# Kernel tuning notes

Measured on AMD Instinct MI355X. Metric: run time of the kernel, lower is better.

Reference implementation:

```python
import jax, jax.numpy as jnp
import numpy as np

E = 1024
H = 4
N = 4096


def _l2norm(x, eps=1e-8):
    n = jnp.linalg.norm(x, axis=-1, keepdims=True)
    return x / jnp.maximum(n, eps)


def mha(q, k, v, in_w, in_b, out_w, out_b):
    # torch nn.MultiheadAttention, unbatched (L, E) inputs, H heads
    d = E // H
    qp = q @ in_w[:E].T + in_b[:E]            # [Lq, E]
    kp = k @ in_w[E:2 * E].T + in_b[E:2 * E]  # [Lk, E]
    vp = v @ in_w[2 * E:].T + in_b[2 * E:]    # [Lk, E]
    qh = qp.reshape(-1, H, d).transpose(1, 0, 2)  # [H, Lq, d]
    kh = kp.reshape(-1, H, d).transpose(1, 0, 2)
    vh = vp.reshape(-1, H, d).transpose(1, 0, 2)
    scores = jnp.einsum('hqd,hkd->hqk', qh, kh) / jnp.sqrt(jnp.asarray(d, qh.dtype))
    attn = jax.nn.softmax(scores, axis=-1)
    oh = jnp.einsum('hqk,hkd->hqd', attn, vh)     # [H, Lq, d]
    o = oh.transpose(1, 0, 2).reshape(-1, E)
    return o @ out_w.T + out_b


def setup_inputs() -> dict:
    key = jax.random.key(0)
    ks = jax.random.split(key, 20)
    f = lambda k, shape, s=1.0: jax.random.normal(k, shape, dtype=jnp.float32) * s
    inp = {
        'local_feat': _l2norm(f(ks[0], (N, E))),
        'global_feat': _l2norm(f(ks[1], (N, E))),
        'text_feat': _l2norm(f(ks[2], (N, E))),
        'pos_emb_local': f(ks[3], (E,), E ** -0.5),
        'pos_emb_global': f(ks[4], (E,), E ** -0.5),
        'fc_w': f(ks[5], (E, E), 0.02), 'fc_b': f(ks[6], (E,), 0.02),
        'lg_in_w': f(ks[7], (3 * E, E), 0.02), 'lg_in_b': f(ks[8], (3 * E,), 0.02),
        'lg_out_w': f(ks[9], (E, E), 0.02), 'lg_out_b': f(ks[10], (E,), 0.02),
        'vt_in_w': f(ks[11], (3 * E, E), 0.02), 'vt_in_b': f(ks[12], (3 * E,), 0.02),
        'vt_out_w': f(ks[13], (E, E), 0.02), 'vt_out_b': f(ks[14], (E,), 0.02),
        'ml_in_w': f(ks[15], (3 * E, E), 0.02), 'ml_in_b': f(ks[16], (3 * E,), 0.02),
        'ml_out_w': f(ks[17], (E, E), 0.02), 'ml_out_b': f(ks[18], (E,), 0.02),
        'quantity': 512,
    }
    return inp


def reference(local_feat, global_feat, text_feat, pos_emb_local, pos_emb_global,
              fc_w, fc_b, lg_in_w, lg_in_b, lg_out_w, lg_out_b,
              vt_in_w, vt_in_b, vt_out_w, vt_out_b,
              ml_in_w, ml_in_b, ml_out_w, ml_out_b, quantity):
    lf = local_feat + pos_emb_local
    gf = global_feat + pos_emb_global
    # local_global
    local_global = mha(lf, gf, gf, lg_in_w, lg_in_b, lg_out_w, lg_out_b) + lf
    # fusion_fc on text (applied fresh in textual_local, textual_global, repeat_text)
    tf = text_feat @ fc_w.T + fc_b
    # textual_local / textual_global (shared fusion_visual_textual weights)
    text_local = mha(tf, lf, lf, vt_in_w, vt_in_b, vt_out_w, vt_out_b) + lf
    text_global = mha(tf, gf, gf, vt_in_w, vt_in_b, vt_out_w, vt_out_b) + tf
    # middle_layer fusions (shared weights)
    gt_gl = mha(local_global, text_global, text_global, ml_in_w, ml_in_b, ml_out_w, ml_out_b)
    gl_lt = mha(text_local, local_global, local_global, ml_in_w, ml_in_b, ml_out_w, ml_out_b)
    full = mha(gl_lt, gt_gl, gt_gl, ml_in_w, ml_in_b, ml_out_w, ml_out_b)
    fusion = mha(tf, full, full, ml_in_w, ml_in_b, ml_out_w, ml_out_b) * tf
    # per-sample cosine-similarity matrices (batched replacement of the .item() loops)
    Q = quantity
    B = N // Q
    ff = _l2norm(fusion.reshape(B, Q, E))
    lb = _l2norm(local_feat.reshape(B, Q, E))
    logits = jnp.einsum('bqe,bke->bqk', ff, lb)  # [B, Q, Q]
    return logits
```

## Files before the change

### kernel.cpp

```cpp
#include <hip/hip_runtime.h>
#include <hip/hip_bf16.h>


typedef __attribute__((ext_vector_type(8))) short short8;
typedef __attribute__((ext_vector_type(4))) float f32x4;
typedef unsigned long long ull;
typedef long long ll;

namespace {
constexpr int NTOK = 4096;
constexpr int EMB  = 1024;
constexpr int QTY  = 512;
}

__device__ __forceinline__ float bf2f(unsigned short u) {
    union { float f; unsigned int i; } x; x.i = ((unsigned int)u) << 16; return x.f;
}
__device__ __forceinline__ unsigned short f2bf(float f) {
    union { float f; unsigned int i; } x; x.f = f;
    unsigned int r = x.i + 0x7fffu + ((x.i >> 16) & 1u);
    return (unsigned short)(r >> 16);
}

#define GLOAD_LDS16(g, l) __builtin_amdgcn_global_load_lds( \
    (const __attribute__((address_space(1))) void*)(g),     \
    (__attribute__((address_space(3))) void*)(l), 16, 0, 0)

template<int SPLITS, int OUTM>
__global__ __launch_bounds__(256)
void gemm_mfma(const unsigned short* __restrict__ Ah, const unsigned short* __restrict__ Al,
               int lda, ll sAz,
               const unsigned short* __restrict__ Bh, const unsigned short* __restrict__ Bl,
               int ldb, ll sBz,
               void* __restrict__ Cp, void* __restrict__ Clp,
               int ldc, ll sCz,
               int K, float alpha, const float* __restrict__ bias, int biasRow,
               const unsigned short* __restrict__ resH, const unsigned short* __restrict__ resL,
               ll sRz, int resMode)
{
    constexpr int NTILES = (SPLITS == 3 ? 4 : (SPLITS == 2 ? 3 : 2));
    constexpr int TSZ = 128 * 32;
    __shared__ unsigned short lds[NTILES * TSZ];
    const int tid  = threadIdx.x;
    const int brow = blockIdx.y * 128;
    const int bcol = blockIdx.x * 128;
    const ll   z   = blockIdx.z;
    Ah += z * sAz; Bh += z * sBz;
    if constexpr (SPLITS == 3) Al += z * sAz;
    if constexpr (SPLITS >= 2) Bl += z * sBz;

    const int lane = tid & 63;
    const int wv = tid >> 6, wr = wv >> 1, wc = wv & 1;
    const int l15 = lane & 15, l4 = lane >> 4;

    f32x4 acc[4][4];
    #pragma unroll
    for (int m = 0; m < 4; ++m)
        #pragma unroll
        for (int n = 0; n < 4; ++n) acc[m][n] = (f32x4){0.f, 0.f, 0.f, 0.f};

    for (int k0 = 0; k0 < K; k0 += 32) {
        #pragma unroll
        for (int i = 0; i < 2; ++i) {
            int idx = tid + i * 256;
            int row = idx >> 2;
            int kc  = (idx & 3) ^ ((row >> 1) & 3);
            GLOAD_LDS16(Ah + (ull)(brow + row) * lda + k0 + kc * 8, &lds[idx * 8]);
            GLOAD_LDS16(Bh + (ull)(bcol + row) * ldb + k0 + kc * 8, &lds[TSZ + idx * 8]);
            if constexpr (SPLITS >= 2)
                GLOAD_LDS16(Bl + (ull)(bcol + row) * ldb + k0 + kc * 8, &lds[2 * TSZ + idx * 8]);
            if constexpr (SPLITS == 3)
                GLOAD_LDS16(Al + (ull)(brow + row) * lda + k0 + kc * 8, &lds[3 * TSZ + idx * 8]);
        }
        __syncthreads();

        short8 ah[4], bh[4], bl2[4], al2[4];
        #pragma unroll
        for (int m = 0; m < 4; ++m) {
            int rr = wr * 64 + m * 16 + l15;
            int sl = l4 ^ ((rr >> 1) & 3);
            int off = rr * 32 + sl * 8;
            ah[m] = *(const short8*)&lds[off];
            if constexpr (SPLITS == 3) al2[m] = *(const short8*)&lds[3 * TSZ + off];
        }
        #pragma unroll
        for (int n = 0; n < 4; ++n) {
            int rr = wc * 64 + n * 16 + l15;
            int sl = l4 ^ ((rr >> 1) & 3);
            int off = rr * 32 + sl * 8;
            bh[n] = *(const short8*)&lds[TSZ + off];
            if constexpr (SPLITS >= 2) bl2[n] = *(const short8*)&lds[2 * TSZ + off];
        }
        #pragma unroll
        for (int m = 0; m < 4; ++m)
            #pragma unroll
            for (int n = 0; n < 4; ++n) {
                acc[m][n] = __builtin_amdgcn_mfma_f32_16x16x32_bf16(ah[m], bh[n], acc[m][n], 0, 0, 0);
                if constexpr (SPLITS >= 2)
                    acc[m][n] = __builtin_amdgcn_mfma_f32_16x16x32_bf16(ah[m], bl2[n], acc[m][n], 0, 0, 0);
                if constexpr (SPLITS == 3)
                    acc[m][n] = __builtin_amdgcn_mfma_f32_16x16x32_bf16(al2[m], bh[n], acc[m][n], 0, 0, 0);
            }
        __syncthreads();
    }

    float* Cf = (float*)Cp + z * sCz;
    unsigned short* Ch = (unsigned short*)Cp + z * sCz;
    unsigned short* Cl = (unsigned short*)Clp + z * sCz;
    const unsigned short* rH = resH + z * sRz;
    const unsigned short* rL = resL + z * sRz;
    const int rowB = brow + wr * 64 + l4 * 4;
    const int colB = bcol + wc * 64 + l15;
    #pragma unroll
    for (int n = 0; n < 4; ++n) {
        int col = colB + n * 16;
        #pragma unroll
        for (int m = 0; m < 4; ++m) {
            #pragma unroll
            for (int r = 0; r < 4; ++r) {
                int row = rowB + m * 16 + r;
                ull ci = (ull)row * ldc + col;
                float v = acc[m][n][r] * alpha;
                if (bias) v += biasRow ? bias[row] : bias[col];
                if (resMode == 1)      v += bf2f(rH[ci]) + bf2f(rL[ci]);
                else if (resMode == 2) v *= bf2f(rH[ci]) + bf2f(rL[ci]);
                if constexpr (OUTM == 0)      Cf[ci] = v;
                else if constexpr (OUTM == 1) Ch[ci] = f2bf(v);
                else {
                    unsigned short h = f2bf(v);
                    Ch[ci] = h;
                    Cl[ci] = f2bf(v - bf2f(h));
                }
            }
        }
    }
}

__global__ __launch_bounds__(256)
void gemm_qkproj(const unsigned short* a0, const unsigned short* a1,
                 const unsigned short* a2, const unsigned short* a3,
                 const unsigned short* __restrict__ W,
                 unsigned short* __restrict__ QK,
                 const float* __restrict__ bias)
{
    constexpr int TSZ = 128 * 32;
    __shared__ unsigned short lds[2 * TSZ];
    const int tid  = threadIdx.x;
    const int brow = blockIdx.y * 128;
    const int bcol = blockIdx.x * 128;
    const int z = blockIdx.z;
    const int j = z & 1, bb = z >> 1;
    const unsigned short* Ah = (z == 0) ? a0 : (z == 1) ? a1 : (z == 2) ? a2 : a3;
    const unsigned short* Bh = W + (ull)j * EMB * EMB;
    unsigned short* C = QK + (ull)bb * NTOK * 2048 + j * 1024;
    const float* bi = bias + j * 1024;

    const int lane = tid & 63;
    const int wv = tid >> 6, wr = wv >> 1, wc = wv & 1;
    const int l15 = lane & 15, l4 = lane >> 4;

    f32x4 acc[4][4];
    #pragma unroll
    for (int m = 0; m < 4; ++m)
        #pragma unroll
        for (int n = 0; n < 4; ++n) acc[m][n] = (f32x4){0.f, 0.f, 0.f, 0.f};

    for (int k0 = 0; k0 < EMB; k0 += 32) {
        #pragma unroll
        for (int i = 0; i < 2; ++i) {
            int idx = tid + i * 256;
            int row = idx >> 2;
            int kc  = (idx & 3) ^ ((row >> 1) & 3);
            GLOAD_LDS16(Ah + (ull)(brow + row) * EMB + k0 + kc * 8, &lds[idx * 8]);
            GLOAD_LDS16(Bh + (ull)(bcol + row) * EMB + k0 + kc * 8, &lds[TSZ + idx * 8]);
        }
        __syncthreads();

        short8 ah[4], bh[4];
        #pragma unroll
        for (int m = 0; m < 4; ++m) {
            int rr = wr * 64 + m * 16 + l15;
            int sl = l4 ^ ((rr >> 1) & 3);
            ah[m] = *(const short8*)&lds[rr * 32 + sl * 8];
        }
        #pragma unroll
        for (int n = 0; n < 4; ++n) {
            int rr = wc * 64 + n * 16 + l15;
            int sl = l4 ^ ((rr >> 1) & 3);
            bh[n] = *(const short8*)&lds[TSZ + rr * 32 + sl * 8];
        }
        #pragma unroll
        for (int m = 0; m < 4; ++m)
            #pragma unroll
            for (int n = 0; n < 4; ++n)
                acc[m][n] = __builtin_amdgcn_mfma_f32_16x16x32_bf16(ah[m], bh[n], acc[m][n], 0, 0, 0);
        __syncthreads();
    }

    const int rowB = brow + wr * 64 + l4 * 4;
    const int colB = bcol + wc * 64 + l15;
    #pragma unroll
    for (int n = 0; n < 4; ++n) {
        int col = colB + n * 16;
        float bv = bi[col];
        #pragma unroll
        for (int m = 0; m < 4; ++m)
            #pragma unroll
            for (int r = 0; r < 4; ++r) {
                int row = rowB + m * 16 + r;
                C[(ull)row * 2048 + col] = f2bf(acc[m][n][r] + bv);
            }
    }
}

template<int NSPLIT>
__global__ __launch_bounds__(512)
void flash_attn(const unsigned short* __restrict__ QK,
                const unsigned short* __restrict__ VT,
                unsigned short* __restrict__ Opart, float* __restrict__ ml,
                unsigned short* __restrict__ attH)
{
    constexpr int KVB = 64;
    constexpr int NTILE = (NTOK / NSPLIT) / KVB;
    __shared__ unsigned short Kt[2][KVB * 256];
    __shared__ unsigned short Vt[2][256 * KVB];

    const int tid = threadIdx.x;
    const int w = tid >> 6, lane = tid & 63;
    const int l15 = lane & 15, l4 = lane >> 4;
    const int qt = blockIdx.x, sp = blockIdx.y;
    const int zb = blockIdx.z, b = zb >> 2, h = zb & 3;
    const int qrow = qt * 128 + w * 16 + l15;
    const int kv0 = sp * (NTOK / NSPLIT);
    const unsigned short* QKb = QK + (ull)b * NTOK * 2048;
    const unsigned short* VTb = VT + (ull)b * 1024 * 4096;

    short8 qreg[8];
    {
        const unsigned short* qp = QKb + (ull)qrow * 2048 + h * 256;
        #pragma unroll
        for (int c = 0; c < 8; ++c) {
            short8 x = *(const short8*)&qp[c * 32 + l4 * 8];
            #pragma unroll
            for (int j = 0; j < 8; ++j)
                x[j] = (short)f2bf(bf2f((unsigned short)x[j]) * 0.0625f);
            qreg[c] = x;
        }
    }

    f32x4 oacc[16];
    #pragma unroll
    for (int dn = 0; dn < 16; ++dn) oacc[dn] = (f32x4){0.f, 0.f, 0.f, 0.f};
    float m_r = -1e30f, l_r = 0.f;

    auto stage = [&](int t, int buf) {
        int base = kv0 + t * KVB;
        #pragma unroll
        for (int i = 0; i < 4; ++i) {
            int s = tid + i * 512;
            int r = s >> 5, c = s & 31;
            int c0 = c ^ (r & 7);
            GLOAD_LDS16(QKb + (ull)(base + r) * 2048 + 1024 + h * 256 + c0 * 8,
                        &Kt[buf][s * 8]);
        }
        #pragma unroll
        for (int i = 0; i < 4; ++i) {
            int s = tid + i * 512;
            int r = s >> 3, c = s & 7;
            int c0 = c ^ (r & 7);
            GLOAD_LDS16(VTb + (ull)(h * 256 + r) * 4096 + base + c0 * 8,
                        &Vt[buf][s * 8]);
        }
    };

    stage(0, 0);
    for (int t = 0; t < NTILE; ++t) {
        if (t + 1 < NTILE) {
            stage(t + 1, (t + 1) & 1);
            asm volatile("s_waitcnt vmcnt(8)");
        } else {
            asm volatile("s_waitcnt vmcnt(0)");
        }
        __builtin_amdgcn_s_barrier();

        const unsigned short* Kb = Kt[t & 1];
        const unsigned short* Vb = Vt[t & 1];

        f32x4 sacc[4];
        #pragma unroll
        for (int fk = 0; fk < 4; ++fk) sacc[fk] = (f32x4){0.f, 0.f, 0.f, 0.f};
        #pragma unroll
        for (int fk = 0; fk < 4; ++fk) {
            int r = fk * 16 + l15;
            int rx = r & 7;
            #pragma unroll
            for (int c = 0; c < 8; ++c) {
                int ch = (4 * c + l4) ^ rx;
                short8 kf = *(const short8*)&Kb[r * 256 + ch * 8];
                sacc[fk] = __builtin_amdgcn_mfma_f32_16x16x32_bf16(kf, qreg[c], sacc[fk], 0, 0, 0);
            }
        }

        float tm = sacc[0][0];
        #pragma unroll
        for (int fk = 0; fk < 4; ++fk)
            #pragma unroll
            for (int rr = 0; rr < 4; ++rr) tm = fmaxf(tm, sacc[fk][rr]);
        tm = fmaxf(tm, __shfl_xor(tm, 16));
        tm = fmaxf(tm, __shfl_xor(tm, 32));

        bool nomax = __all(tm <= m_r);
        float mnew = nomax ? m_r : fmaxf(m_r, tm);
        if (!nomax) {
            float corr = __expf(m_r - mnew);
            float c4[4];
            #pragma unroll
            for (int r = 0; r < 4; ++r) c4[r] = __shfl(corr, l4 * 4 + r);
            #pragma unroll
            for (int dn = 0; dn < 16; ++dn)
                #pragma unroll
                for (int r = 0; r < 4; ++r) oacc[dn][r] *= c4[r];
            l_r *= corr;
            m_r = mnew;
        }

        float p[16]; float ls = 0.f;
        #pragma unroll
        for (int fk = 0; fk < 4; ++fk)
            #pragma unroll
            for (int rr = 0; rr < 4; ++rr) {
                float e = __expf(sacc[fk][rr] - m_r);
                p[fk * 4 + rr] = e; ls += e;
            }
        ls += __shfl_xor(ls, 16);
        ls += __shfl_xor(ls, 32);
        l_r += ls;

        unsigned int W[4][2];
        #pragma unroll
        for (int f = 0; f < 4; ++f)
            #pragma unroll
            for (int pp = 0; pp < 2; ++pp)
                W[f][pp] = (unsigned int)f2bf(p[f * 4 + 2 * pp]) |
                           ((unsigned int)f2bf(p[f * 4 + 2 * pp + 1]) << 16);

        const int sbase = l15 + ((l4 & 1) << 5);
        const bool hi = (l4 >> 1) & 1;
        #pragma unroll
        for (int kvc = 0; kvc < 2; ++kvc) {
            unsigned int a0 = (unsigned int)__shfl((int)W[2 * kvc][0], sbase);
            unsigned int a1 = (unsigned int)__shfl((int)W[2 * kvc][1], sbase);
            unsigned int a2 = (unsigned int)__shfl((int)W[2 * kvc][0], sbase + 16);
            unsigned int a3 = (unsigned int)__shfl((int)W[2 * kvc][1], sbase + 16);
            unsigned int b0 = (unsigned int)__shfl((int)W[2 * kvc + 1][0], sbase);
            unsigned int b1 = (unsigned int)__shfl((int)W[2 * kvc + 1][1], sbase);
            unsigned int b2 = (unsigned int)__shfl((int)W[2 * kvc + 1][0], sbase + 16);
            unsigned int b3 = (unsigned int)__shfl((int)W[2 * kvc + 1][1], sbase + 16);
            union { unsigned int u[4]; short8 s8; } pa;
            pa.u[0] = hi ? b0 : a0; pa.u[1] = hi ? b1 : a1;
            pa.u[2] = hi ? b2 : a2; pa.u[3] = hi ? b3 : a3;

            #pragma unroll
            for (int dn = 0; dn < 16; ++dn) {
                int row = dn * 16 + l15;
                int ch = (kvc * 4 + l4) ^ (row & 7);
                short8 vf = *(const short8*)&Vb[row * 64 + ch * 8];
                oacc[dn] = __builtin_amdgcn_mfma_f32_16x16x32_bf16(pa.s8, vf, oacc[dn], 0, 0, 0);
            }
        }
        __builtin_amdgcn_s_barrier();
    }

    float inv = 1.f / l_r;
    float i4[4];
    #pragma unroll
    for (int r = 0; r < 4; ++r) i4[r] = __shfl(inv, l4 * 4 + r);

    if constexpr (NSPLIT == 2) {
        unsigned short* Ob = Opart + (((ull)b * 2 + sp) * 4 + h) * NTOK * 256;
        #pragma unroll
        for (int dn = 0; dn < 16; ++dn) {
            int d = dn * 16 + l15;
            #pragma unroll
            for (int r = 0; r < 4; ++r) {
                int q = qt * 128 + w * 16 + l4 * 4 + r;
                Ob[(ull)q * 256 + d] = f2bf(oacc[dn][r] * i4[r]);
            }
        }
        if (l4 == 0) {
            float2* mlp = (float2*)ml + (((ull)b * 2 + sp) * 4 + h) * NTOK + qrow;
            *mlp = make_float2(m_r, l_r);
        }
    } else {
        unsigned short* Ob = attH + (ull)b * NTOK * EMB;
        #pragma unroll
        for (int dn = 0; dn < 16; ++dn) {
            int d = dn * 16 + l15;
            #pragma unroll
            for (int r = 0; r < 4; ++r) {
                int q = qt * 128 + w * 16 + l4 * 4 + r;
                Ob[(ull)q * EMB + h * 256 + d] = f2bf(oacc[dn][r] * i4[r]);
            }
        }
    }
}

__global__ __launch_bounds__(256)
void flash_combine(const unsigned short* __restrict__ Opart, const float* __restrict__ ml,
                   unsigned short* __restrict__ attH)
{
    const int bx = blockIdx.x;
    const int b = bx >> 12, q = bx & 4095;
    const int t = threadIdx.x;
    const int h = t >> 6, d4 = (t & 63) * 4;

    float2 m0 = ((const float2*)ml)[(((ull)b * 2 + 0) * 4 + h) * NTOK + q];
    float2 m1 = ((const float2*)ml)[(((ull)b * 2 + 1) * 4 + h) * NTOK + q];
    float ms = fmaxf(m0.x, m1.x);
    float w0 = __expf(m0.x - ms) * m0.y;
    float w1 = __expf(m1.x - ms) * m1.y;
    float inv = 1.f / (w0 + w1);
    w0 *= inv; w1 *= inv;

    ushort4 o0 = *(const ushort4*)&Opart[((((ull)b * 2 + 0) * 4 + h) * NTOK + q) * 256 + d4];
    ushort4 o1 = *(const ushort4*)&Opart[((((ull)b * 2 + 1) * 4 + h) * NTOK + q) * 256 + d4];
    ushort4 ho;
    ho.x = f2bf(w0 * bf2f(o0.x) + w1 * bf2f(o1.x));
    ho.y = f2bf(w0 * bf2f(o0.y) + w1 * bf2f(o1.y));
    ho.z = f2bf(w0 * bf2f(o0.z) + w1 * bf2f(o1.z));
    ho.w = f2bf(w0 * bf2f(o0.w) + w1 * bf2f(o1.w));
    *(ushort4*)&attH[(ull)b * NTOK * EMB + (ull)q * EMB + h * 256 + d4] = ho;
}

template<bool F32IN>
__global__ __launch_bounds__(256)
void l2norm_rows(const float* __restrict__ inF, const unsigned short* __restrict__ inH,
                 const unsigned short* __restrict__ inL,
                 unsigned short* __restrict__ oH, unsigned short* __restrict__ oL)
{
    const ull row = blockIdx.x;
    const int t = threadIdx.x;
    const int lane = t & 63, wid = t >> 6;
    __shared__ float red[4];

    float v[4];
    if constexpr (F32IN) {
        float4 x = *(const float4*)&inF[row * EMB + t * 4];
        v[0] = x.x; v[1] = x.y; v[2] = x.z; v[3] = x.w;
    } else {
        ushort4 hh = *(const ushort4*)&inH[row * EMB + t * 4];
        ushort4 ll2 = *(const ushort4*)&inL[row * EMB + t * 4];
        v[0] = bf2f(hh.x) + bf2f(ll2.x); v[1] = bf2f(hh.y) + bf2f(ll2.y);
        v[2] = bf2f(hh.z) + bf2f(ll2.z); v[3] = bf2f(hh.w) + bf2f(ll2.w);
    }
    float ss = v[0] * v[0] + v[1] * v[1] + v[2] * v[2] + v[3] * v[3];
    #pragma unroll
    for (int o = 32; o > 0; o >>= 1) ss += __shfl_down(ss, o);
    if (lane == 0) red[wid] = ss;
    __syncthreads();
    ss = red[0] + red[1] + red[2] + red[3];

    float inv = 1.f / fmaxf(sqrtf(ss), 1e-8f);
    ushort4 ho, lo;
    float s0 = v[0] * inv, s1 = v[1] * inv, s2 = v[2] * inv, s3 = v[3] * inv;
    ho.x = f2bf(s0); lo.x = f2bf(s0 - bf2f(ho.x));
    ho.y = f2bf(s1); lo.y = f2bf(s1 - bf2f(ho.y));
    ho.z = f2bf(s2); lo.z = f2bf(s2 - bf2f(ho.z));
    ho.w = f2bf(s3); lo.w = f2bf(s3 - bf2f(ho.w));
    *(ushort4*)&oH[row * EMB + t * 4] = ho;
    *(ushort4*)&oL[row * EMB + t * 4] = lo;
}

__global__ __launch_bounds__(256)
void add_pos_pair(const float* __restrict__ in, const float* __restrict__ pos,
                  unsigned short* __restrict__ oH, unsigned short* __restrict__ oL)
{
    ull i = ((ull)blockIdx.x * 256 + threadIdx.x) * 4;
    float4 a = *(const float4*)&in[i];
    float4 p = *(const float4*)&pos[(int)(i & (EMB - 1))];
    float w[4] = { a.x + p.x, a.y + p.y, a.z + p.z, a.w + p.w };
    ushort4 ho, lo;
    ho.x = f2bf(w[0]); lo.x = f2bf(w[0] - bf2f(ho.x));
    ho.y = f2bf(w[1]); lo.y = f2bf(w[1] - bf2f(ho.y));
    ho.z = f2bf(w[2]); lo.z = f2bf(w[2] - bf2f(ho.z));
    ho.w = f2bf(w[3]); lo.w = f2bf(w[3] - bf2f(ho.w));
    *(ushort4*)&oH[i] = ho;
    *(ushort4*)&oL[i] = lo;
}

__global__ __launch_bounds__(256)
void split_pair(const float* __restrict__ in, unsigned short* __restrict__ oH,
                unsigned short* __restrict__ oL)
{
    ull i = ((ull)blockIdx.x * 256 + threadIdx.x) * 4;
    float4 a = *(const float4*)&in[i];
    float w[4] = { a.x, a.y, a.z, a.w };
    ushort4 ho, lo;
    ho.x = f2bf(w[0]); lo.x = f2bf(w[0] - bf2f(ho.x));
    ho.y = f2bf(w[1]); lo.y = f2bf(w[1] - bf2f(ho.y));
    ho.z = f2bf(w[2]); lo.z = f2bf(w[2] - bf2f(ho.z));
    ho.w = f2bf(w[3]); lo.w = f2bf(w[3] - bf2f(ho.w));
    *(ushort4*)&oH[i] = ho;
    *(ushort4*)&oL[i] = lo;
}

__global__ __launch_bounds__(256)
void cast_bf16(const float* __restrict__ in, unsigned short* __restrict__ out)
{
    ull i = ((ull)blockIdx.x * 256 + threadIdx.x) * 4;
    float4 a = *(const float4*)&in[i];
    ushort4 ho;
    ho.x = f2bf(a.x); ho.y = f2bf(a.y); ho.z = f2bf(a.z); ho.w = f2bf(a.w);
    *(ushort4*)&out[i] = ho;
}

namespace {

template<int S, int O>
inline void G(dim3 grid,
              const unsigned short* Ah, const unsigned short* Al, int lda, ll sAz,
              const unsigned short* Bh, const unsigned short* Bl, int ldb, ll sBz,
              void* Ch, void* Cl, int ldc, ll sCz,
              int K, float alpha, const float* bias, int biasRow,
              const unsigned short* rh, const unsigned short* rl, ll sRz, int rm,
              hipStream_t st)
{
    gemm_mfma<S, O><<<grid, dim3(256), 0, st>>>(Ah, Al, lda, sAz, Bh, Bl, ldb, sBz,
                                                Ch, Cl, ldc, sCz, K, alpha, bias, biasRow,
                                                rh, rl, sRz, rm);
}

struct Bufs {
    unsigned short *Ph[6], *Pl[6];
    unsigned short *ATTh, *QK, *VT, *Wih, *Woh, *Wol, *Opart;
    float *ml;
};

void run_mha(int batch,
             const unsigned short* qh, ll sQ,
             const unsigned short* kh, ll sK,
             const float* in_w, const float* in_b,
             const float* out_w, const float* out_b,
             unsigned short* dsth, unsigned short* dstl,
             const unsigned short* resh, const unsigned short* resl, ll sR, int resMode,
             const Bufs& B, bool convW, hipStream_t s)
{
    const ull EE = (ull)EMB * EMB;
    const ll  TE = (ll)NTOK * EMB;
    const ll  VTBS = (ll)1024 * 4096;
    if (convW) {
        cast_bf16<<<3 * EE / 1024, 256, 0, s>>>(in_w, B.Wih);
        split_pair<<<EE / 1024, 256, 0, s>>>(out_w, B.Woh, B.Wol);
    }
    gemm_qkproj<<<dim3(8, 32, 2 * batch), 256, 0, s>>>(
        qh, kh, qh + sQ, kh + sK, B.Wih, B.QK, in_b);
    G<1, 1>(dim3(32, 8, batch), B.Wih + 2 * EE, nullptr, EMB, 0, kh, nullptr, EMB, sK,
            B.VT, nullptr, 4096, VTBS, EMB, 1.f, in_b + 2 * EMB, 1, nullptr, nullptr, 0, 0, s);

    if (batch == 1) {
        flash_attn<2><<<dim3(32, 2, 4), 512, 0, s>>>(B.QK, B.VT, B.Opart, B.ml, B.ATTh);
        flash_combine<<<NTOK, 256, 0, s>>>(B.Opart, B.ml, B.ATTh);
    } else {
        flash_attn<1><<<dim3(32, 1, 4 * batch), 512, 0, s>>>(B.QK, B.VT, B.Opart, B.ml, B.ATTh);
    }

    G<2, 2>(dim3(8, 32, batch), B.ATTh, nullptr, EMB, TE, B.Woh, B.Wol, EMB, 0,
            dsth, dstl, EMB, 2 * TE, EMB, 1.f, out_b, 0, resh, resl, sR, resMode, s);
}

}

extern "C" void kernel_launch(void* const* d_in, const int* in_sizes, int n_in,
                              void* d_out, int out_size, void* d_ws, size_t ws_size,
                              hipStream_t stream) {
    const float* local_feat  = (const float*)d_in[0];
    const float* global_feat = (const float*)d_in[1];
    const float* text_feat   = (const float*)d_in[2];
    const float* pos_l       = (const float*)d_in[3];
    const float* pos_g       = (const float*)d_in[4];
    const float* fc_w        = (const float*)d_in[5];
    const float* fc_b        = (const float*)d_in[6];
    const float* lg_in_w     = (const float*)d_in[7];
    const float* lg_in_b     = (const float*)d_in[8];
    const float* lg_out_w    = (const float*)d_in[9];
    const float* lg_out_b    = (const float*)d_in[10];
    const float* vt_in_w     = (const float*)d_in[11];
    const float* vt_in_b     = (const float*)d_in[12];
    const float* vt_out_w    = (const float*)d_in[13];
    const float* vt_out_b    = (const float*)d_in[14];
    const float* ml_in_w     = (const float*)d_in[15];
    const float* ml_in_b     = (const float*)d_in[16];
    const float* ml_out_w    = (const float*)d_in[17];
    const float* ml_out_b    = (const float*)d_in[18];
    float* out = (float*)d_out;

    const ull TE = (ull)NTOK * EMB;
    const ull EE = (ull)EMB * EMB;
    unsigned short* w = (unsigned short*)d_ws;
    Bufs B;
    for (int i = 0; i < 6; ++i) { B.Ph[i] = w + (2 * i) * TE; B.Pl[i] = w + (2 * i + 1) * TE; }
    B.ATTh  = w + 12 * TE;
    B.QK    = w + 14 * TE;
    B.VT    = w + 18 * TE;
    B.Opart = w + 20 * TE;
    B.ml    = (float*)(w + 24 * TE);
    B.Wih   = w + 25 * TE;
    B.Woh   = B.Wih + 3 * EE;
    B.Wol   = B.Woh + EE;

    add_pos_pair<<<TE / 1024, 256, 0, stream>>>(local_feat, pos_l, B.Ph[0], B.Pl[0]);
    add_pos_pair<<<TE / 1024, 256, 0, stream>>>(global_feat, pos_g, B.Ph[1], B.Pl[1]);

    split_pair<<<TE / 1024, 256, 0, stream>>>(text_feat, B.QK, B.QK + TE);
    split_pair<<<EE / 1024, 256, 0, stream>>>(fc_w, B.Woh, B.Wol);
    G<3, 2>(dim3(EMB / 128, NTOK / 128), B.QK, B.QK + TE, EMB, 0, B.Woh, B.Wol, EMB, 0,
            B.Ph[2], B.Pl[2], EMB, 0, EMB, 1.f, fc_b, 0, nullptr, nullptr, 0, 0, stream);

    const ll T2 = (ll)2 * TE, T4 = (ll)4 * TE;
    run_mha(1, B.Ph[0], 0, B.Ph[1], 0, lg_in_w, lg_in_b, lg_out_w, lg_out_b,
            B.Ph[3], B.Pl[3], B.Ph[0], B.Pl[0], 0, 1, B, true, stream);
    run_mha(2, B.Ph[2], 0, B.Ph[0], T2, vt_in_w, vt_in_b, vt_out_w, vt_out_b,
            B.Ph[4], B.Pl[4], B.Ph[0], B.Pl[0], T4, 1, B, true, stream);
    run_mha(2, B.Ph[3], T2, B.Ph[5], -T4, ml_in_w, ml_in_b, ml_out_w, ml_out_b,
            B.Ph[0], B.Pl[0], nullptr, nullptr, 0, 0, B, true, stream);
    run_mha(1, B.Ph[1], 0, B.Ph[0], 0, ml_in_w, ml_in_b, ml_out_w, ml_out_b,
            B.Ph[3], B.Pl[3], nullptr, nullptr, 0, 0, B, false, stream);
    run_mha(1, B.Ph[2], 0, B.Ph[3], 0, ml_in_w, ml_in_b, ml_out_w, ml_out_b,
            B.Ph[4], B.Pl[4], B.Ph[2], B.Pl[2], 0, 2, B, false, stream);

    l2norm_rows<false><<<NTOK, 256, 0, stream>>>(nullptr, B.Ph[4], B.Pl[4], B.Ph[4], B.Pl[4]);
    l2norm_rows<true ><<<NTOK, 256, 0, stream>>>(local_feat, nullptr, nullptr, B.Ph[5], B.Pl[5]);

    G<3, 0>(dim3(QTY / 128, QTY / 128, 8),
            B.Ph[4], B.Pl[4], EMB, (ll)QTY * EMB,
            B.Ph[5], B.Pl[5], EMB, (ll)QTY * EMB,
            out, nullptr, QTY, (ll)QTY * QTY,
            EMB, 1.f, nullptr, 0, nullptr, nullptr, 0, 0, stream);
}
```

Baseline: 1.687 ms.

## Give each flash-attention wave two query fragments, smaller KV tiles, and more KV splits

```diff
diff --git a/kernel.cpp b/kernel.cpp
--- a/kernel.cpp
+++ b/kernel.cpp
@@ -214,13 +214,12 @@
 }
 
 template<int NSPLIT>
-__global__ __launch_bounds__(512)
+__global__ __launch_bounds__(256, 1)
 void flash_attn(const unsigned short* __restrict__ QK,
                 const unsigned short* __restrict__ VT,
-                unsigned short* __restrict__ Opart, float* __restrict__ ml,
-                unsigned short* __restrict__ attH)
-{
-    constexpr int KVB = 64;
+                unsigned short* __restrict__ Opart, float* __restrict__ ml)
+{
+    constexpr int KVB = 32;
     constexpr int NTILE = (NTOK / NSPLIT) / KVB;
     __shared__ unsigned short Kt[2][KVB * 256];
     __shared__ unsigned short Vt[2][256 * KVB];
@@ -230,34 +229,37 @@
     const int l15 = lane & 15, l4 = lane >> 4;
     const int qt = blockIdx.x, sp = blockIdx.y;
     const int zb = blockIdx.z, b = zb >> 2, h = zb & 3;
-    const int qrow = qt * 128 + w * 16 + l15;
+    const int qbase = qt * 128 + w * 32;
     const int kv0 = sp * (NTOK / NSPLIT);
     const unsigned short* QKb = QK + (ull)b * NTOK * 2048;
     const unsigned short* VTb = VT + (ull)b * 1024 * 4096;
 
-    short8 qreg[8];
-    {
-        const unsigned short* qp = QKb + (ull)qrow * 2048 + h * 256;
+    short8 qreg[2][8];
+    #pragma unroll
+    for (int qf = 0; qf < 2; ++qf) {
+        const unsigned short* qp = QKb + (ull)(qbase + qf * 16 + l15) * 2048 + h * 256;
         #pragma unroll
         for (int c = 0; c < 8; ++c) {
             short8 x = *(const short8*)&qp[c * 32 + l4 * 8];
             #pragma unroll
             for (int j = 0; j < 8; ++j)
                 x[j] = (short)f2bf(bf2f((unsigned short)x[j]) * 0.0625f);
-            qreg[c] = x;
-        }
-    }
-
-    f32x4 oacc[16];
-    #pragma unroll
-    for (int dn = 0; dn < 16; ++dn) oacc[dn] = (f32x4){0.f, 0.f, 0.f, 0.f};
-    float m_r = -1e30f, l_r = 0.f;
+            qreg[qf][c] = x;
+        }
+    }
+
+    f32x4 oacc[2][16];
+    #pragma unroll
+    for (int qf = 0; qf < 2; ++qf)
+        #pragma unroll
+        for (int dn = 0; dn < 16; ++dn) oacc[qf][dn] = (f32x4){0.f, 0.f, 0.f, 0.f};
+    float m_r[2] = { -1e30f, -1e30f }, l_r[2] = { 0.f, 0.f };
 
     auto stage = [&](int t, int buf) {
         int base = kv0 + t * KVB;
         #pragma unroll
         for (int i = 0; i < 4; ++i) {
-            int s = tid + i * 512;
+            int s = tid + i * 256;
             int r = s >> 5, c = s & 31;
             int c0 = c ^ (r & 7);
             GLOAD_LDS16(QKb + (ull)(base + r) * 2048 + 1024 + h * 256 + c0 * 8,
@@ -265,9 +267,9 @@
         }
         #pragma unroll
         for (int i = 0; i < 4; ++i) {
-            int s = tid + i * 512;
-            int r = s >> 3, c = s & 7;
-            int c0 = c ^ (r & 7);
+            int s = tid + i * 256;
+            int r = s >> 2, c = s & 3;
+            int c0 = c ^ (r & 3);
             GLOAD_LDS16(VTb + (ull)(h * 256 + r) * 4096 + base + c0 * 8,
                         &Vt[buf][s * 8]);
         }
@@ -286,125 +288,124 @@
         const unsigned short* Kb = Kt[t & 1];
         const unsigned short* Vb = Vt[t & 1];
 
-        f32x4 sacc[4];
-        #pragma unroll
-        for (int fk = 0; fk < 4; ++fk) sacc[fk] = (f32x4){0.f, 0.f, 0.f, 0.f};
-        #pragma unroll
-        for (int fk = 0; fk < 4; ++fk) {
+        f32x4 sacc[2][2];
+        #pragma unroll
+        for (int qf = 0; qf < 2; ++qf)
+            #pragma unroll
+            for (int fk = 0; fk < 2; ++fk) sacc[qf][fk] = (f32x4){0.f, 0.f, 0.f, 0.f};
+
+        #pragma unroll
+        for (int fk = 0; fk < 2; ++fk) {
             int r = fk * 16 + l15;
             int rx = r & 7;
             #pragma unroll
             for (int c = 0; c < 8; ++c) {
                 int ch = (4 * c + l4) ^ rx;
                 short8 kf = *(const short8*)&Kb[r * 256 + ch * 8];
-                sacc[fk] = __builtin_amdgcn_mfma_f32_16x16x32_bf16(kf, qreg[c], sacc[fk], 0, 0, 0);
+                sacc[0][fk] = __builtin_amdgcn_mfma_f32_16x16x32_bf16(kf, qreg[0][c], sacc[0][fk], 0, 0, 0);
+                sacc[1][fk] = __builtin_amdgcn_mfma_f32_16x16x32_bf16(kf, qreg[1][c], sacc[1][fk], 0, 0, 0);
             }
         }
 
-        float tm = sacc[0][0];
-        #pragma unroll
-        for (int fk = 0; fk < 4; ++fk)
-            #pragma unroll
-            for (int rr = 0; rr < 4; ++rr) tm = fmaxf(tm, sacc[fk][rr]);
-        tm = fmaxf(tm, __shfl_xor(tm, 16));
-        tm = fmaxf(tm, __shfl_xor(tm, 32));
-
-        bool nomax = __all(tm <= m_r);
-        float mnew = nomax ? m_r : fmaxf(m_r, tm);
-        if (!nomax) {
-            float corr = __expf(m_r - mnew);
-            float c4[4];
-            #pragma unroll
-            for (int r = 0; r < 4; ++r) c4[r] = __shfl(corr, l4 * 4 + r);
-            #pragma unroll
-            for (int dn = 0; dn < 16; ++dn)
+        unsigned int W[2][2][2];
+        #pragma unroll
+        for (int qf = 0; qf < 2; ++qf) {
+            float tm = sacc[qf][0][0];
+            #pragma unroll
+            for (int fk = 0; fk < 2; ++fk)
                 #pragma unroll
-                for (int r = 0; r < 4; ++r) oacc[dn][r] *= c4[r];
-            l_r *= corr;
-            m_r = mnew;
-        }
-
-        float p[16]; float ls = 0.f;
-        #pragma unroll
-        for (int fk = 0; fk < 4; ++fk)
-            #pragma unroll
-            for (int rr = 0; rr < 4; ++rr) {
-                float e = __expf(sacc[fk][rr] - m_r);
-                p[fk * 4 + rr] = e; ls += e;
+                for (int rr = 0; rr < 4; ++rr) tm = fmaxf(tm, sacc[qf][fk][rr]);
+            tm = fmaxf(tm, __shfl_xor(tm, 16));
+            tm = fmaxf(tm, __shfl_xor(tm, 32));
+
+            bool nomax = __all(tm <= m_r[qf]);
+            float mnew = nomax ? m_r[qf] : fmaxf(m_r[qf], tm);
+            if (!nomax) {
+                float corr = __expf(m_r[qf] - mnew);
+                float c4[4];
+                #pragma unroll
+                for (int r = 0; r < 4; ++r) c4[r] = __shfl(corr, l4 * 4 + r);
+                #pragma unroll
+                for (int dn = 0; dn < 16; ++dn)
+                    #pragma unroll
+                    for (int r = 0; r < 4; ++r) oacc[qf][dn][r] *= c4[r];
+                l_r[qf] *= corr;
+                m_r[qf] = mnew;
             }
-        ls += __shfl_xor(ls, 16);
-        ls += __shfl_xor(ls, 32);
-        l_r += ls;
-
-        unsigned int W[4][2];
-        #pragma unroll
-        for (int f = 0; f < 4; ++f)
-            #pragma unroll
-            for (int pp = 0; pp < 2; ++pp)
-                W[f][pp] = (unsigned int)f2bf(p[f * 4 + 2 * pp]) |
-                           ((unsigned int)f2bf(p[f * 4 + 2 * pp + 1]) << 16);
+
+            float ls = 0.f;
+            #pragma unroll
+            for (int fk = 0; fk < 2; ++fk)
+                #pragma unroll
+                for (int rr = 0; rr < 4; ++rr) {
+                    float e = __expf(sacc[qf][fk][rr] - m_r[qf]);
+                    sacc[qf][fk][rr] = e; ls += e;
+                }
+            ls += __shfl_xor(ls, 16);
+            ls += __shfl_xor(ls, 32);
+            l_r[qf] += ls;
+
+            #pragma unroll
+            for (int fk = 0; fk < 2; ++fk)
+                #pragma unroll
+                for (int pp = 0; pp < 2; ++pp)
+                    W[qf][fk][pp] = (unsigned int)f2bf(sacc[qf][fk][2 * pp]) |
+                                    ((unsigned int)f2bf(sacc[qf][fk][2 * pp + 1]) << 16);
+        }
 
         const int sbase = l15 + ((l4 & 1) << 5);
         const bool hi = (l4 >> 1) & 1;
-        #pragma unroll
-        for (int kvc = 0; kvc < 2; ++kvc) {
-            unsigned int a0 = (unsigned int)__shfl((int)W[2 * kvc][0], sbase);
-            unsigned int a1 = (unsigned int)__shfl((int)W[2 * kvc][1], sbase);
-            unsigned int a2 = (unsigned int)__shfl((int)W[2 * kvc][0], sbase + 16);
-            unsigned int a3 = (unsigned int)__shfl((int)W[2 * kvc][1], sbase + 16);
-            unsigned int b0 = (unsigned int)__shfl((int)W[2 * kvc + 1][0], sbase);
-            unsigned int b1 = (unsigned int)__shfl((int)W[2 * kvc + 1][1], sbase);
-            unsigned int b2 = (unsigned int)__shfl((int)W[2 * kvc + 1][0], sbase + 16);
-            unsigned int b3 = (unsigned int)__shfl((int)W[2 * kvc + 1][1], sbase + 16);
-            union { unsigned int u[4]; short8 s8; } pa;
-            pa.u[0] = hi ? b0 : a0; pa.u[1] = hi ? b1 : a1;
-            pa.u[2] = hi ? b2 : a2; pa.u[3] = hi ? b3 : a3;
-
-            #pragma unroll
-            for (int dn = 0; dn < 16; ++dn) {
-                int row = dn * 16 + l15;
-                int ch = (kvc * 4 + l4) ^ (row & 7);
-                short8 vf = *(const short8*)&Vb[row * 64 + ch * 8];
-                oacc[dn] = __builtin_amdgcn_mfma_f32_16x16x32_bf16(pa.s8, vf, oacc[dn], 0, 0, 0);
-            }
+        union { unsigned int u[4]; short8 s8; } pa[2];
+        #pragma unroll
+        for (int qf = 0; qf < 2; ++qf) {
+            unsigned int a0 = (unsigned int)__shfl((int)W[qf][0][0], sbase);
+            unsigned int a1 = (unsigned int)__shfl((int)W[qf][0][1], sbase);
+            unsigned int a2 = (unsigned int)__shfl((int)W[qf][0][0], sbase + 16);
+            unsigned int a3 = (unsigned int)__shfl((int)W[qf][0][1], sbase + 16);
+            unsigned int b0 = (unsigned int)__shfl((int)W[qf][1][0], sbase);
+            unsigned int b1 = (unsigned int)__shfl((int)W[qf][1][1], sbase);
+            unsigned int b2 = (unsigned int)__shfl((int)W[qf][1][0], sbase + 16);
+            unsigned int b3 = (unsigned int)__shfl((int)W[qf][1][1], sbase + 16);
+            pa[qf].u[0] = hi ? b0 : a0; pa[qf].u[1] = hi ? b1 : a1;
+            pa[qf].u[2] = hi ? b2 : a2; pa[qf].u[3] = hi ? b3 : a3;
+        }
+
+        #pragma unroll
+        for (int dn = 0; dn < 16; ++dn) {
+            int row = dn * 16 + l15;
+            int ch = l4 ^ (row & 3);
+            short8 vf = *(const short8*)&Vb[row * 32 + ch * 8];
+            oacc[0][dn] = __builtin_amdgcn_mfma_f32_16x16x32_bf16(pa[0].s8, vf, oacc[0][dn], 0, 0, 0);
+            oacc[1][dn] = __builtin_amdgcn_mfma_f32_16x16x32_bf16(pa[1].s8, vf, oacc[1][dn], 0, 0, 0);
         }
         __builtin_amdgcn_s_barrier();
     }
 
-    float inv = 1.f / l_r;
-    float i4[4];
-    #pragma unroll
-    for (int r = 0; r < 4; ++r) i4[r] = __shfl(inv, l4 * 4 + r);
-
-    if constexpr (NSPLIT == 2) {
-        unsigned short* Ob = Opart + (((ull)b * 2 + sp) * 4 + h) * NTOK * 256;
+    unsigned short* Ob = Opart + (((ull)b * NSPLIT + sp) * 4 + h) * NTOK * 256;
+    #pragma unroll
+    for (int qf = 0; qf < 2; ++qf) {
+        float inv = 1.f / l_r[qf];
+        float i4[4];
+        #pragma unroll
+        for (int r = 0; r < 4; ++r) i4[r] = __shfl(inv, l4 * 4 + r);
         #pragma unroll
         for (int dn = 0; dn < 16; ++dn) {
             int d = dn * 16 + l15;
             #pragma unroll
             for (int r = 0; r < 4; ++r) {
-                int q = qt * 128 + w * 16 + l4 * 4 + r;
-                Ob[(ull)q * 256 + d] = f2bf(oacc[dn][r] * i4[r]);
+                int q = qbase + qf * 16 + l4 * 4 + r;
+                Ob[(ull)q * 256 + d] = f2bf(oacc[qf][dn][r] * i4[r]);
             }
         }
         if (l4 == 0) {
-            float2* mlp = (float2*)ml + (((ull)b * 2 + sp) * 4 + h) * NTOK + qrow;
-            *mlp = make_float2(m_r, l_r);
-        }
-    } else {
-        unsigned short* Ob = attH + (ull)b * NTOK * EMB;
-        #pragma unroll
-        for (int dn = 0; dn < 16; ++dn) {
-            int d = dn * 16 + l15;
-            #pragma unroll
-            for (int r = 0; r < 4; ++r) {
-                int q = qt * 128 + w * 16 + l4 * 4 + r;
-                Ob[(ull)q * EMB + h * 256 + d] = f2bf(oacc[dn][r] * i4[r]);
-            }
-        }
-    }
-}
-
+            float2* mlp = (float2*)ml + (((ull)b * NSPLIT + sp) * 4 + h) * NTOK
+                          + qbase + qf * 16 + l15;
+            *mlp = make_float2(m_r[qf], l_r[qf]);
+        }
+    }
+}
+
+template<int NS>
 __global__ __launch_bounds__(256)
 void flash_combine(const unsigned short* __restrict__ Opart, const float* __restrict__ ml,
                    unsigned short* __restrict__ attH)
@@ -414,21 +415,29 @@
     const int t = threadIdx.x;
     const int h = t >> 6, d4 = (t & 63) * 4;
 
-    float2 m0 = ((const float2*)ml)[(((ull)b * 2 + 0) * 4 + h) * NTOK + q];
-    float2 m1 = ((const float2*)ml)[(((ull)b * 2 + 1) * 4 + h) * NTOK + q];
-    float ms = fmaxf(m0.x, m1.x);
-    float w0 = __expf(m0.x - ms) * m0.y;
-    float w1 = __expf(m1.x - ms) * m1.y;
-    float inv = 1.f / (w0 + w1);
-    w0 *= inv; w1 *= inv;
-
-    ushort4 o0 = *(const ushort4*)&Opart[((((ull)b * 2 + 0) * 4 + h) * NTOK + q) * 256 + d4];
-    ushort4 o1 = *(const ushort4*)&Opart[((((ull)b * 2 + 1) * 4 + h) * NTOK + q) * 256 + d4];
+    float2 ms_[NS]; float mmax = -1e30f;
+    #pragma unroll
+    for (int s = 0; s < NS; ++s) {
+        ms_[s] = ((const float2*)ml)[(((ull)b * NS + s) * 4 + h) * NTOK + q];
+        mmax = fmaxf(mmax, ms_[s].x);
+    }
+    float wt[NS], denom = 0.f;
+    #pragma unroll
+    for (int s = 0; s < NS; ++s) {
+        wt[s] = __expf(ms_[s].x - mmax) * ms_[s].y;
+        denom += wt[s];
+    }
+    float inv = 1.f / denom;
+    float acc[4] = { 0.f, 0.f, 0.f, 0.f };
+    #pragma unroll
+    for (int s = 0; s < NS; ++s) {
+        ushort4 o = *(const ushort4*)&Opart[((((ull)b * NS + s) * 4 + h) * NTOK + q) * 256 + d4];
+        acc[0] += wt[s] * bf2f(o.x); acc[1] += wt[s] * bf2f(o.y);
+        acc[2] += wt[s] * bf2f(o.z); acc[3] += wt[s] * bf2f(o.w);
+    }
     ushort4 ho;
-    ho.x = f2bf(w0 * bf2f(o0.x) + w1 * bf2f(o1.x));
-    ho.y = f2bf(w0 * bf2f(o0.y) + w1 * bf2f(o1.y));
-    ho.z = f2bf(w0 * bf2f(o0.z) + w1 * bf2f(o1.z));
-    ho.w = f2bf(w0 * bf2f(o0.w) + w1 * bf2f(o1.w));
+    ho.x = f2bf(acc[0] * inv); ho.y = f2bf(acc[1] * inv);
+    ho.z = f2bf(acc[2] * inv); ho.w = f2bf(acc[3] * inv);
     *(ushort4*)&attH[(ull)b * NTOK * EMB + (ull)q * EMB + h * 256 + d4] = ho;
 }
 
@@ -558,10 +567,11 @@
             B.VT, nullptr, 4096, VTBS, EMB, 1.f, in_b + 2 * EMB, 1, nullptr, nullptr, 0, 0, s);
 
     if (batch == 1) {
-        flash_attn<2><<<dim3(32, 2, 4), 512, 0, s>>>(B.QK, B.VT, B.Opart, B.ml, B.ATTh);
-        flash_combine<<<NTOK, 256, 0, s>>>(B.Opart, B.ml, B.ATTh);
+        flash_attn<4><<<dim3(32, 4, 4), 256, 0, s>>>(B.QK, B.VT, B.Opart, B.ml);
+        flash_combine<4><<<NTOK, 256, 0, s>>>(B.Opart, B.ml, B.ATTh);
     } else {
-        flash_attn<1><<<dim3(32, 1, 4 * batch), 512, 0, s>>>(B.QK, B.VT, B.Opart, B.ml, B.ATTh);
+        flash_attn<2><<<dim3(32, 2, 4 * batch), 256, 0, s>>>(B.QK, B.VT, B.Opart, B.ml);
+        flash_combine<2><<<batch * NTOK, 256, 0, s>>>(B.Opart, B.ml, B.ATTh);
     }
 
     G<2, 2>(dim3(8, 32, batch), B.ATTh, nullptr, EMB, TE, B.Woh, B.Wol, EMB, 0,
```

Measured after the change: 2.081 ms. 1.23x slower.
